# Kernel tuning notes

Hardware: AMD Instinct MI355X
Metric: run time of the kernel (lower is better)

The kernel has to match this reference:

```python
import jax, jax.numpy as jnp
import numpy as np

# Layer widths of the hardcoded torch MLP: 2->128->256->512->512->512->512->256->128->3
_DIMS = [2, 128, 256, 512, 512, 512, 512, 256, 128, 3]


def setup_inputs() -> dict:
    key = jax.random.key(0)
    keys = jax.random.split(key, 2 * (len(_DIMS) - 1) + 1)
    inp = {"x": jax.random.uniform(keys[0], (1048576, 2), dtype=jnp.float32)}
    for i in range(len(_DIMS) - 1):
        fan_in, fan_out = _DIMS[i], _DIMS[i + 1]
        bound = 1.0 / np.sqrt(fan_in)  # torch nn.Linear default init range
        inp[f"W{i+1}"] = jax.random.uniform(keys[2 * i + 1], (fan_in, fan_out), jnp.float32, -bound, bound)
        inp[f"b{i+1}"] = jax.random.uniform(keys[2 * i + 2], (fan_out,), jnp.float32, -bound, bound)
    return inp


def reference(x, W1, b1, W2, b2, W3, b3, W4, b4, W5, b5, W6, b6, W7, b7, W8, b8, W9, b9):
    # (transpose of torch's [out, in]); math is identical: y = x @ W + b.
    h = x
    for W, b in ((W1, b1), (W2, b2), (W3, b3), (W4, b4),
                 (W5, b5), (W6, b6), (W7, b7), (W8, b8)):
        h = jax.nn.relu(h @ W + b)
    return jax.nn.sigmoid(h @ W9 + b9)
```

## Files before the change

kernel.cpp:

```cpp
#include <hip/hip_runtime.h>

typedef _Float16 f16;
typedef __attribute__((ext_vector_type(4))) _Float16 f16x4;
typedef __attribute__((ext_vector_type(8))) _Float16 f16x8;
typedef __attribute__((ext_vector_type(16))) float f32x16;

#define MT 128
#define NBF 4
#define LDSP 1024

#define OFF2 0
#define OFF3 32768
#define OFF4 163840
#define OFF5 425984
#define OFF6 688128
#define OFF7 950272
#define OFF8 1081344
#define OFF9 1114112
#define TOTAL_FRAG_LANES 139776

__device__ __forceinline__ uint32_t swz(int row, int colbytes) {
  return (uint32_t)(row * LDSP + (colbytes ^ ((row & 31) << 4)));
}

__global__ void repack_kernel(const float* __restrict__ W2, const float* __restrict__ W3,
                              const float* __restrict__ W4, const float* __restrict__ W5,
                              const float* __restrict__ W6, const float* __restrict__ W7,
                              const float* __restrict__ W8, const float* __restrict__ W9,
                              f16* __restrict__ ws) {
  int gid = blockIdx.x * 256 + threadIdx.x;
  if (gid >= TOTAL_FRAG_LANES) return;
  const float* src; int N, NT; size_t dst; int local;
  if      (gid <   4096) { src = W2; N = 256; NT = 8;  dst = OFF2; local = gid;          }
  else if (gid <  20480) { src = W3; N = 512; NT = 16; dst = OFF3; local = gid -   4096; }
  else if (gid <  53248) { src = W4; N = 512; NT = 16; dst = OFF4; local = gid -  20480; }
  else if (gid <  86016) { src = W5; N = 512; NT = 16; dst = OFF5; local = gid -  53248; }
  else if (gid < 118784) { src = W6; N = 512; NT = 16; dst = OFF6; local = gid -  86016; }
  else if (gid < 135168) { src = W7; N = 256; NT = 8;  dst = OFF7; local = gid - 118784; }
  else if (gid < 139264) { src = W8; N = 128; NT = 4;  dst = OFF8; local = gid - 135168; }
  else                   { src = W9; N = 3;   NT = 1;  dst = OFF9; local = gid - 139264; }
  int lane = local & 63;
  int frag = local >> 6;
  int kf = frag / NT, nf = frag % NT;
  int n  = nf * 32 + (lane & 31);
  int kb = kf * 16 + ((lane >> 5) << 3);
  f16x8 v;
  #pragma unroll
  for (int i = 0; i < 8; ++i) {
    float val = (n < N) ? src[(size_t)(kb + i) * N + n] : 0.0f;
    v[i] = (f16)val;
  }
  *reinterpret_cast<f16x8*>(ws + dst + (size_t)local * 8) = v;
}

template<int KT, int MF, int WMG, int WBG>
__device__ __forceinline__ void run_layer(char* act, const f16* __restrict__ wp,
                                          const float* __restrict__ bias) {
  constexpr int FM  = MF / WMG;
  constexpr int FB  = NBF / WBG;
  const int tid   = threadIdx.x;
  const int lane  = tid & 63;
  const int wid   = tid >> 6;
  const int wm    = wid / WBG;
  const int wb    = wid % WBG;
  const int mlane = lane & 31;
  const int h     = lane >> 5;

  f32x16 acc[FM][FB];
  #pragma unroll
  for (int fm = 0; fm < FM; ++fm) {
    const int mbase = (wm * FM + fm) * 32;
    #pragma unroll
    for (int g = 0; g < 4; ++g) {
      const float4 bb = *reinterpret_cast<const float4*>(&bias[mbase + g * 8 + 4 * h]);
      #pragma unroll
      for (int j = 0; j < 4; ++j)
        #pragma unroll
        for (int fb = 0; fb < FB; ++fb)
          acc[fm][fb][g * 4 + j] = ((const float*)&bb)[j];
    }
  }

  const f16x8* __restrict__ wfrag = reinterpret_cast<const f16x8*>(wp);

  #pragma unroll 2
  for (int kf = 0; kf < KT; ++kf) {
    f16x8 a[FM];
    #pragma unroll
    for (int fm = 0; fm < FM; ++fm)
      a[fm] = wfrag[(size_t)(kf * MF + wm * FM + fm) * 64 + lane];
    f16x8 b[FB];
    #pragma unroll
    for (int fb = 0; fb < FB; ++fb)
      b[fb] = *reinterpret_cast<const f16x8*>(
                  act + swz((wb * FB + fb) * 32 + mlane, kf * 32 + h * 16));
    #pragma unroll
    for (int fm = 0; fm < FM; ++fm)
      #pragma unroll
      for (int fb = 0; fb < FB; ++fb)
        acc[fm][fb] = __builtin_amdgcn_mfma_f32_32x32x16_f16(a[fm], b[fb], acc[fm][fb], 0, 0, 0);
  }

  __syncthreads();
  #pragma unroll
  for (int fm = 0; fm < FM; ++fm) {
    const int mbase = (wm * FM + fm) * 32;
    #pragma unroll
    for (int fb = 0; fb < FB; ++fb) {
      const int row = (wb * FB + fb) * 32 + mlane;
      #pragma unroll
      for (int g = 0; g < 4; ++g) {
        const int m0 = mbase + g * 8 + 4 * h;
        f16x4 v;
        #pragma unroll
        for (int j = 0; j < 4; ++j)
          v[j] = (f16)fmaxf(acc[fm][fb][g * 4 + j], 0.0f);
        *reinterpret_cast<f16x4*>(act + swz(row, m0 * 2)) = v;
      }
    }
  }
  __syncthreads();
}

__global__ __launch_bounds__(512, 2)
void mlp_kernel(const float* __restrict__ x,
                const float* __restrict__ W1, const float* __restrict__ b1,
                const f16*   __restrict__ wpk,
                const float* __restrict__ b2, const float* __restrict__ b3,
                const float* __restrict__ b4, const float* __restrict__ b5,
                const float* __restrict__ b6, const float* __restrict__ b7,
                const float* __restrict__ b8, const float* __restrict__ b9,
                float* __restrict__ out) {
  __shared__ __align__(16) char act[MT * LDSP];
  const int row0 = blockIdx.x * MT;
  const int tid  = threadIdx.x;

  {
    const int r  = tid >> 2;
    const int cb = (tid & 3) * 32;
    const float2 xv = reinterpret_cast<const float2*>(x)[row0 + r];
    #pragma unroll
    for (int q = 0; q < 4; ++q) {
      f16x8 v;
      #pragma unroll
      for (int j = 0; j < 8; ++j) {
        int c = cb + q * 8 + j;
        v[j] = (f16)fmaxf(fmaf(xv.y, W1[128 + c], fmaf(xv.x, W1[c], b1[c])), 0.0f);
      }
      *reinterpret_cast<f16x8*>(act + swz(r, cb * 2 + q * 16)) = v;
    }
  }
  __syncthreads();

  run_layer<8,  8,  8, 1>(act, wpk + OFF2, b2);
  run_layer<16, 16, 8, 1>(act, wpk + OFF3, b3);
  run_layer<32, 16, 8, 1>(act, wpk + OFF4, b4);
  run_layer<32, 16, 8, 1>(act, wpk + OFF5, b5);
  run_layer<32, 16, 8, 1>(act, wpk + OFF6, b6);
  run_layer<32, 8,  8, 1>(act, wpk + OFF7, b7);
  run_layer<16, 4,  4, 2>(act, wpk + OFF8, b8);

  const int lane = tid & 63;
  const int wid  = tid >> 6;
  if (wid < 4) {
    const int mlane = lane & 31;
    const int h     = lane >> 5;
    f32x16 acc = (f32x16)0.0f;
    const f16x8* __restrict__ wfrag = reinterpret_cast<const f16x8*>(wpk + OFF9);
    #pragma unroll
    for (int kf = 0; kf < 8; ++kf) {
      f16x8 a = wfrag[(size_t)kf * 64 + lane];
      f16x8 b = *reinterpret_cast<const f16x8*>(
                    act + swz(wid * 32 + mlane, kf * 32 + h * 16));
      acc = __builtin_amdgcn_mfma_f32_32x32x16_f16(a, b, acc, 0, 0, 0);
    }
    if (h == 0) {
      const size_t orow = (size_t)(row0 + wid * 32 + mlane) * 3;
      #pragma unroll
      for (int r = 0; r < 3; ++r) {
        float v = acc[r] + b9[r];
        out[orow + r] = 1.0f / (1.0f + __expf(-v));
      }
    }
  }
}

extern "C" void kernel_launch(void* const* d_in, const int* in_sizes, int n_in,
                              void* d_out, int out_size, void* d_ws, size_t ws_size,
                              hipStream_t stream) {
  const float* x  = (const float*)d_in[0];
  const float* W1 = (const float*)d_in[1];  const float* b1 = (const float*)d_in[2];
  const float* W2 = (const float*)d_in[3];  const float* b2 = (const float*)d_in[4];
  const float* W3 = (const float*)d_in[5];  const float* b3 = (const float*)d_in[6];
  const float* W4 = (const float*)d_in[7];  const float* b4 = (const float*)d_in[8];
  const float* W5 = (const float*)d_in[9];  const float* b5 = (const float*)d_in[10];
  const float* W6 = (const float*)d_in[11]; const float* b6 = (const float*)d_in[12];
  const float* W7 = (const float*)d_in[13]; const float* b7 = (const float*)d_in[14];
  const float* W8 = (const float*)d_in[15]; const float* b8 = (const float*)d_in[16];
  const float* W9 = (const float*)d_in[17]; const float* b9 = (const float*)d_in[18];
  f16* wpk = (f16*)d_ws;

  repack_kernel<<<(TOTAL_FRAG_LANES + 255) / 256, 256, 0, stream>>>(
      W2, W3, W4, W5, W6, W7, W8, W9, wpk);

  mlp_kernel<<<1048576 / MT, 512, 0, stream>>>(
      x, W1, b1, wpk, b2, b3, b4, b5, b6, b7, b8, b9, (float*)d_out);
}
```

Baseline: 2.063 ms.

## Stream layer weights into per-wave LDS ring via async global_load_lds with cross-layer prefetch

Replaces direct global loads of weight fragments in layers 2-7 with a per-wave double-buffered LDS ring filled by global_load_lds, prefetching two steps ahead, including the first steps of the next layer. Activation reads are software-pipelined in registers, and MFMA groups are wrapped in s_setprio. The aim is to hide global and L2 latency of the weight stream behind MFMA work. It adds 32KB of LDS per block, which may reduce occupancy from 2 blocks per CU, and relies on hand-placed waitcnt counts.

```diff
diff --git a/kernel.cpp b/kernel.cpp
--- a/kernel.cpp
+++ b/kernel.cpp
@@ -8,6 +8,7 @@
 #define MT 128
 #define NBF 4
 #define LDSP 1024
+#define RING_B 32768
 
 #define OFF2 0
 #define OFF3 32768
@@ -53,18 +54,139 @@
   *reinterpret_cast<f16x8*>(ws + dst + (size_t)local * 8) = v;
 }
 
+__device__ __forceinline__ void gload16(const f16* g, char* l) {
+  __builtin_amdgcn_global_load_lds(
+      (const __attribute__((address_space(1))) void*)g,
+      (__attribute__((address_space(3))) void*)l, 16, 0, 0);
+}
+
+template<int MF>
+__device__ __forceinline__ void stage_step(const f16* __restrict__ wp, int t,
+                                           char* ringwave, int wid, int lane) {
+  constexpr int KPS = 16 / MF;
+  char* dst = ringwave + ((t & 1) << 11);
+  int g0, g1;
+  if constexpr (MF == 16) { g0 = t * 16 + wid * 2;       g1 = g0 + 1; }
+  else                    { g0 = (t * KPS) * MF + wid;   g1 = (t * KPS + 1) * MF + wid; }
+  gload16(wp + (size_t)g0 * 512 + (size_t)lane * 8, dst);
+  gload16(wp + (size_t)g1 * 512 + (size_t)lane * 8, dst + 1024);
+}
+
+template<int KT, int MF, int NXT_MF, bool STAGE_NEXT>
+__device__ __forceinline__ void run_staged(char* act, char* ring,
+    const f16* __restrict__ wp, const f16* __restrict__ wp_next,
+    const float* __restrict__ bias, int tid, f16x8& wc0, f16x8& wc1) {
+  constexpr int FM = MF / 8, KPS = 16 / MF, NS = (KT * MF) / 16, BN = KPS * 4;
+  const int lane = tid & 63, wid = tid >> 6;
+  const int mlane = lane & 31, h = lane >> 5;
+  char* ringwave = ring + (wid << 12);
+  const uint32_t l16 = (uint32_t)lane * 16;
+
+  f32x16 acc[FM][4];
+  #pragma unroll
+  for (int fm = 0; fm < FM; ++fm) {
+    const int mbase = (wid * FM + fm) * 32;
+    #pragma unroll
+    for (int g = 0; g < 4; ++g) {
+      const float4 bb = *reinterpret_cast<const float4*>(&bias[mbase + g * 8 + 4 * h]);
+      #pragma unroll
+      for (int j = 0; j < 4; ++j)
+        #pragma unroll
+        for (int fb = 0; fb < 4; ++fb)
+          acc[fm][fb][g * 4 + j] = ((const float*)&bb)[j];
+    }
+  }
+
+  uint32_t rbase[4], rx[4];
+  #pragma unroll
+  for (int fb = 0; fb < 4; ++fb) {
+    int row = fb * 32 + mlane;
+    rbase[fb] = (uint32_t)row * LDSP;
+    rx[fb] = (uint32_t)((row & 31) << 4);
+  }
+
+  f16x8 cw0 = wc0, cw1 = wc1, nw0, nw1;
+  f16x8 cb[BN], nb[BN];
+  #pragma unroll
+  for (int kk = 0; kk < KPS; ++kk)
+    #pragma unroll
+    for (int fb = 0; fb < 4; ++fb)
+      cb[kk * 4 + fb] = *reinterpret_cast<const f16x8*>(
+          act + rbase[fb] + ((uint32_t)(kk * 32 + h * 16) ^ rx[fb]));
+
+#define STEP(S, CW0, CW1, CB, NW0, NW1, NB, DOSTAGE, WAIT0, DOREAD)            \
+  {                                                                            \
+    asm volatile("s_waitcnt lgkmcnt(0)" ::: "memory");                         \
+    if constexpr (DOSTAGE) {                                                   \
+      if ((S) + 2 < NS) stage_step<MF>(wp, (S) + 2, ringwave, wid, lane);      \
+      else stage_step<NXT_MF>(wp_next, (S) + 2 - NS, ringwave, wid, lane);     \
+    }                                                                          \
+    __builtin_amdgcn_s_setprio(1);                                             \
+    _Pragma("unroll")                                                          \
+    for (int fb = 0; fb < 4; ++fb)                                             \
+      acc[0][fb] = __builtin_amdgcn_mfma_f32_32x32x16_f16(CW0, CB[fb], acc[0][fb], 0, 0, 0); \
+    __builtin_amdgcn_s_setprio(0);                                             \
+    if constexpr (WAIT0) { asm volatile("s_waitcnt vmcnt(0)" ::: "memory"); }  \
+    else                 { asm volatile("s_waitcnt vmcnt(2)" ::: "memory"); }  \
+    if constexpr (DOREAD) {                                                    \
+      const char* slot = ringwave + ((((S) + 1) & 1) << 11);                   \
+      NW0 = *reinterpret_cast<const f16x8*>(slot + l16);                       \
+      NW1 = *reinterpret_cast<const f16x8*>(slot + 1024 + l16);                \
+      _Pragma("unroll")                                                        \
+      for (int kk = 0; kk < KPS; ++kk)                                         \
+        _Pragma("unroll")                                                      \
+        for (int fb = 0; fb < 4; ++fb)                                         \
+          NB[kk * 4 + fb] = *reinterpret_cast<const f16x8*>(                   \
+              act + rbase[fb] + ((uint32_t)((((S) + 1) * KPS + kk) * 32 + h * 16) ^ rx[fb])); \
+    }                                                                          \
+    __builtin_amdgcn_s_setprio(1);                                             \
+    _Pragma("unroll")                                                          \
+    for (int fb = 0; fb < 4; ++fb)                                             \
+      acc[FM - 1][fb] = __builtin_amdgcn_mfma_f32_32x32x16_f16(CW1, CB[BN - 4 + fb], acc[FM - 1][fb], 0, 0, 0); \
+    __builtin_amdgcn_s_setprio(0);                                             \
+  }
+
+  constexpr int STEADY = STAGE_NEXT ? NS : NS - 2;
+  #pragma unroll 1
+  for (int s = 0; s < STEADY; s += 2) {
+    STEP(s,     cw0, cw1, cb, nw0, nw1, nb, true, false, true)
+    STEP(s + 1, nw0, nw1, nb, cw0, cw1, cb, true, false, true)
+  }
+  if constexpr (!STAGE_NEXT) {
+    STEP(NS - 2, cw0, cw1, cb, nw0, nw1, nb, false, true, true)
+    STEP(NS - 1, nw0, nw1, nb, cw0, cw1, cb, false, true, false)
+  }
+#undef STEP
+  wc0 = cw0; wc1 = cw1;
+
+  __syncthreads();
+  #pragma unroll
+  for (int fm = 0; fm < FM; ++fm) {
+    const int mbase = (wid * FM + fm) * 32;
+    #pragma unroll
+    for (int fb = 0; fb < 4; ++fb) {
+      const int row = fb * 32 + mlane;
+      #pragma unroll
+      for (int g = 0; g < 4; ++g) {
+        const int m0 = mbase + g * 8 + 4 * h;
+        f16x4 v;
+        #pragma unroll
+        for (int j = 0; j < 4; ++j)
+          v[j] = (f16)fmaxf(acc[fm][fb][g * 4 + j], 0.0f);
+        *reinterpret_cast<f16x4*>(act + swz(row, m0 * 2)) = v;
+      }
+    }
+  }
+  __syncthreads();
+}
+
 template<int KT, int MF, int WMG, int WBG>
-__device__ __forceinline__ void run_layer(char* act, const f16* __restrict__ wp,
-                                          const float* __restrict__ bias) {
-  constexpr int FM  = MF / WMG;
-  constexpr int FB  = NBF / WBG;
-  const int tid   = threadIdx.x;
-  const int lane  = tid & 63;
-  const int wid   = tid >> 6;
-  const int wm    = wid / WBG;
-  const int wb    = wid % WBG;
-  const int mlane = lane & 31;
-  const int h     = lane >> 5;
+__device__ __forceinline__ void run_direct(char* act, const f16* __restrict__ wp,
+                                           const float* __restrict__ bias, int tid) {
+  constexpr int FM = MF / WMG, FB = NBF / WBG;
+  const int lane = tid & 63, wid = tid >> 6;
+  const int wm = wid / WBG, wb = wid % WBG;
+  const int mlane = lane & 31, h = lane >> 5;
 
   f32x16 acc[FM][FB];
   #pragma unroll
@@ -80,9 +202,7 @@
           acc[fm][fb][g * 4 + j] = ((const float*)&bb)[j];
     }
   }
-
   const f16x8* __restrict__ wfrag = reinterpret_cast<const f16x8*>(wp);
-
   #pragma unroll 2
   for (int kf = 0; kf < KT; ++kf) {
     f16x8 a[FM];
@@ -93,14 +213,13 @@
     #pragma unroll
     for (int fb = 0; fb < FB; ++fb)
       b[fb] = *reinterpret_cast<const f16x8*>(
-                  act + swz((wb * FB + fb) * 32 + mlane, kf * 32 + h * 16));
+          act + swz((wb * FB + fb) * 32 + mlane, kf * 32 + h * 16));
     #pragma unroll
     for (int fm = 0; fm < FM; ++fm)
       #pragma unroll
       for (int fb = 0; fb < FB; ++fb)
         acc[fm][fb] = __builtin_amdgcn_mfma_f32_32x32x16_f16(a[fm], b[fb], acc[fm][fb], 0, 0, 0);
   }
-
   __syncthreads();
   #pragma unroll
   for (int fm = 0; fm < FM; ++fm) {
@@ -132,8 +251,14 @@
                 const float* __restrict__ b8, const float* __restrict__ b9,
                 float* __restrict__ out) {
   __shared__ __align__(16) char act[MT * LDSP];
+  __shared__ __align__(16) char ring[RING_B];
   const int row0 = blockIdx.x * MT;
   const int tid  = threadIdx.x;
+  const int lane = tid & 63, wid = tid >> 6;
+  char* ringwave = ring + (wid << 12);
+
+  stage_step<8>(wpk + OFF2, 0, ringwave, wid, lane);
+  stage_step<8>(wpk + OFF2, 1, ringwave, wid, lane);
 
   {
     const int r  = tid >> 2;
@@ -152,16 +277,20 @@
   }
   __syncthreads();
 
-  run_layer<8,  8,  8, 1>(act, wpk + OFF2, b2);
-  run_layer<16, 16, 8, 1>(act, wpk + OFF3, b3);
-  run_layer<32, 16, 8, 1>(act, wpk + OFF4, b4);
-  run_layer<32, 16, 8, 1>(act, wpk + OFF5, b5);
-  run_layer<32, 16, 8, 1>(act, wpk + OFF6, b6);
-  run_layer<32, 8,  8, 1>(act, wpk + OFF7, b7);
-  run_layer<16, 4,  4, 2>(act, wpk + OFF8, b8);
-
-  const int lane = tid & 63;
-  const int wid  = tid >> 6;
+  f16x8 wc0 = *reinterpret_cast<const f16x8*>(ringwave + (uint32_t)lane * 16);
+  f16x8 wc1 = *reinterpret_cast<const f16x8*>(ringwave + 1024 + (uint32_t)lane * 16);
+
+  run_staged<8,  8,  16, true >(act, ring, wpk + OFF2, wpk + OFF3, b2, tid, wc0, wc1);
+  run_staged<16, 16, 16, true >(act, ring, wpk + OFF3, wpk + OFF4, b3, tid, wc0, wc1);
+  #pragma unroll 1
+  for (int rep = 0; rep < 2; ++rep)
+    run_staged<32, 16, 16, true>(act, ring, wpk + OFF4 + rep * (OFF5 - OFF4),
+                                 wpk + OFF5 + rep * (OFF5 - OFF4),
+                                 (rep == 0) ? b4 : b5, tid, wc0, wc1);
+  run_staged<32, 16, 8,  true >(act, ring, wpk + OFF6, wpk + OFF7, b6, tid, wc0, wc1);
+  run_staged<32, 8,  8,  false>(act, ring, wpk + OFF7, wpk,        b7, tid, wc0, wc1);
+  run_direct<16, 4, 4, 2>(act, wpk + OFF8, b8, tid);
+
   if (wid < 4) {
     const int mlane = lane & 31;
     const int h     = lane >> 5;
@@ -171,7 +300,7 @@
     for (int kf = 0; kf < 8; ++kf) {
       f16x8 a = wfrag[(size_t)kf * 64 + lane];
       f16x8 b = *reinterpret_cast<const f16x8*>(
-                    act + swz(wid * 32 + mlane, kf * 32 + h * 16));
+          act + swz(wid * 32 + mlane, kf * 32 + h * 16));
       acc = __builtin_amdgcn_mfma_f32_32x32x16_f16(a, b, acc, 0, 0, 0);
     }
     if (h == 0) {
```

Result: no change. 2.103 ms (+1.9%).
